# Kernel optimization log

Hardware: AMD Instinct MI355X
Metric: run time of the kernel (lower is better)

## Reference

```python
import jax, jax.numpy as jnp
import numpy as np

N = 100000
E = 1600000
IN_C = 128
HID = 32
H1 = 4
OUT_C = 32
H2 = 1
NEG_SLOPE = 0.2


def setup_inputs() -> dict:
    key = jax.random.key(0)
    ks = jax.random.split(key, 12)
    g = 0.1  # glorot-ish scale
    return {
        "x": jax.random.normal(ks[0], (N, IN_C), jnp.float32),
        "edge_index": jax.random.randint(ks[1], (2, E), 0, N, jnp.int64),
        "W1": jax.random.normal(ks[2], (IN_C, H1 * HID), jnp.float32) * g,
        "att_src1": jax.random.normal(ks[3], (H1, HID), jnp.float32) * g,
        "att_dst1": jax.random.normal(ks[4], (H1, HID), jnp.float32) * g,
        "b1": jnp.zeros((H1 * HID,), jnp.float32),
        "W2": jax.random.normal(ks[5], (H1 * HID, H2 * OUT_C), jnp.float32) * g,
        "att_src2": jax.random.normal(ks[6], (H2, OUT_C), jnp.float32) * g,
        "att_dst2": jax.random.normal(ks[7], (H2, OUT_C), jnp.float32) * g,
        "b2": jnp.zeros((H2 * OUT_C,), jnp.float32),
    }


def gat_conv(x, src, dst, W, att_src, att_dst, bias, heads, ch):
    n = x.shape[0]
    h = (x @ W).reshape(n, heads, ch)                      # [N,H,C]
    a_src = jnp.sum(h * att_src, axis=-1)                  # [N,H]
    a_dst = jnp.sum(h * att_dst, axis=-1)                  # [N,H]
    e = jax.nn.leaky_relu(a_src[src] + a_dst[dst], NEG_SLOPE)  # [E,H]
    # segment softmax over destination neighborhoods
    m = jax.ops.segment_max(e, dst, num_segments=n)        # [N,H]
    ex = jnp.exp(e - m[dst])
    denom = jax.ops.segment_sum(ex, dst, num_segments=n)   # [N,H]
    alpha = ex / (denom[dst] + 1e-16)                      # [E,H]
    msg = h[src] * alpha[:, :, None]                       # [E,H,C]
    out = jax.ops.segment_sum(msg, dst, num_segments=n)    # [N,H,C]
    return out.reshape(n, heads * ch) + bias


def reference(x, edge_index, W1, att_src1, att_dst1, b1, W2, att_src2, att_dst2, b2):
    # PyG GATConv add_self_loops=True
    loops = jnp.arange(N, dtype=edge_index.dtype)
    src = jnp.concatenate([edge_index[0], loops])
    dst = jnp.concatenate([edge_index[1], loops])
    # dropout is a no-op at inference
    h = gat_conv(x, src, dst, W1, att_src1, att_dst1, b1, H1, HID)
    h = jax.nn.relu(h)
    out = gat_conv(h, src, dst, W2, att_src2, att_dst2, b2, H2, OUT_C)
    return out
```

## Files before the change

### kernel.cpp

```cpp
#include <hip/hip_runtime.h>
#include <hip/hip_bf16.h>


#define NSLOPE 0.2f
#define GSTRIDE 136
#define NB_MAX 400
#define CHUNK 4096
#define CAP 5632

typedef __attribute__((ext_vector_type(8))) short short8;
typedef __attribute__((ext_vector_type(4))) float floatx4;

__device__ __forceinline__ float leaky(float v) { return v > 0.f ? v : NSLOPE * v; }

__device__ __forceinline__ unsigned short f2bf(float f) {
  __hip_bfloat16 b = __float2bfloat16(f);
  return *reinterpret_cast<unsigned short*>(&b);
}
__device__ __forceinline__ float bf2f(unsigned int u) {
  return __uint_as_float(u << 16);
}
__device__ __forceinline__ unsigned int pack2(float a, float b) {
  return (unsigned int)f2bf(a) | ((unsigned int)f2bf(b) << 16);
}

__global__ __launch_bounds__(256, 2) void fused1_kernel(
    const float* __restrict__ x, const float* __restrict__ W,
    const float* __restrict__ atts, const float* __restrict__ attd,
    unsigned short* __restrict__ h, float* __restrict__ asrc, float* __restrict__ adst,
    int n, int g1blocks,
    const int* __restrict__ ei, int* __restrict__ bincur,
    unsigned int* __restrict__ staging, int E, int ET, int nb) {
  __shared__ __align__(16) unsigned char smem[70656];
  const int tid = threadIdx.x;

  if (blockIdx.x < g1blocks) {
    unsigned short* xs = (unsigned short*)smem;
    unsigned short* wt = (unsigned short*)(smem + 34816);
    float* att_s = (float*)(smem + 69632);
    float* att_d = (float*)(smem + 70144);
    const int row0 = blockIdx.x * 128;

    if (tid < 128) { att_s[tid] = atts[tid]; att_d[tid] = attd[tid]; }

    const float4* w4 = (const float4*)W;
#pragma unroll
    for (int i = 0; i < 16; i++) {
      int idx = tid + i * 256;
      int k = idx >> 5, n0 = (idx & 31) * 4;
      float4 v = w4[idx];
      float vv[4] = {v.x, v.y, v.z, v.w};
#pragma unroll
      for (int jj = 0; jj < 4; jj++) {
        int j = (jj + tid) & 3;
        wt[(n0 + j) * GSTRIDE + k] = f2bf(vv[j]);
      }
    }

    const float4* x4 = (const float4*)x;
#pragma unroll
    for (int i = 0; i < 16; i++) {
      int idx = tid + i * 256;
      int r = idx >> 5, c4 = idx & 31;
      float4 v = make_float4(0.f, 0.f, 0.f, 0.f);
      if (row0 + r < n) v = x4[(size_t)(row0 + r) * 32 + c4];
      unsigned int* p = (unsigned int*)&xs[r * GSTRIDE + c4 * 4];
      p[0] = pack2(v.x, v.y);
      p[1] = pack2(v.z, v.w);
    }
    __syncthreads();

    const int l = tid & 63;
    const int w = tid >> 6;
    const int mrow = l & 15;
    const int q = l >> 4;
    floatx4 acc[2][8];
#pragma unroll
    for (int mt = 0; mt < 2; mt++)
#pragma unroll
      for (int nt = 0; nt < 8; nt++) acc[mt][nt] = (floatx4){0.f, 0.f, 0.f, 0.f};

#pragma unroll
    for (int ks = 0; ks < 4; ks++) {
      const int k0 = ks * 32 + q * 8;
      short8 a0 = *(const short8*)&xs[(w * 32 + mrow) * GSTRIDE + k0];
      short8 a1 = *(const short8*)&xs[(w * 32 + 16 + mrow) * GSTRIDE + k0];
#pragma unroll
      for (int nt = 0; nt < 8; nt++) {
        short8 b = *(const short8*)&wt[(nt * 16 + mrow) * GSTRIDE + k0];
        acc[0][nt] = __builtin_amdgcn_mfma_f32_16x16x32_bf16(a0, b, acc[0][nt], 0, 0, 0);
        acc[1][nt] = __builtin_amdgcn_mfma_f32_16x16x32_bf16(a1, b, acc[1][nt], 0, 0, 0);
      }
    }
    __syncthreads();

#pragma unroll
    for (int mt = 0; mt < 2; mt++)
#pragma unroll
      for (int nt = 0; nt < 8; nt++)
#pragma unroll
        for (int i = 0; i < 4; i++) {
          int r = w * 32 + mt * 16 + q * 4 + i;
          xs[r * GSTRIDE + nt * 16 + mrow] = f2bf(acc[mt][nt][i]);
        }
    __syncthreads();

#pragma unroll
    for (int i = 0; i < 8; i++) {
      int idx = tid + i * 256;
      int r = idx >> 4, c8 = (idx & 15) * 8;
      if (row0 + r < n) {
        unsigned int* p = (unsigned int*)&xs[r * GSTRIDE + c8];
        uint4 v = make_uint4(p[0], p[1], p[2], p[3]);
        *(uint4*)(h + (size_t)(row0 + r) * 128 + c8) = v;
      }
    }

#pragma unroll
    for (int rr = 0; rr < 2; rr++) {
      int row = (tid >> 2) + rr * 64;
      int head = tid & 3;
      float ss = 0.f, sd = 0.f;
#pragma unroll
      for (int c = 0; c < 32; c++) {
        int cr = (c + tid) & 31;
        float hv = bf2f(xs[row * GSTRIDE + head * 32 + cr]);
        ss += hv * att_s[head * 32 + cr];
        sd += hv * att_d[head * 32 + cr];
      }
      if (row0 + row < n) {
        asrc[(size_t)(row0 + row) * 4 + head] = ss;
        adst[(size_t)(row0 + row) * 4 + head] = sd;
      }
    }
  } else {
    int* hist  = (int*)smem;
    int* run   = (int*)(smem + 1600);
    int* rbase = (int*)(smem + 3200);
    const int base = (blockIdx.x - g1blocks) * CHUNK;
    for (int i = tid; i < nb; i += 256) { hist[i] = 0; run[i] = 0; }
    __syncthreads();
    int se[16], de[16];
#pragma unroll
    for (int j = 0; j < 16; j++) {
      int idx = base + j * 256 + tid;
      if (idx < ET) {
        if (idx < E) { se[j] = ei[idx]; de[j] = ei[E + idx]; }
        else         { se[j] = de[j] = idx - E; }
        atomicAdd(&hist[de[j] >> 8], 1);
      } else de[j] = -1;
    }
    __syncthreads();
    for (int i = tid; i < nb; i += 256)
      rbase[i] = hist[i] ? (i * CAP + atomicAdd(&bincur[i], hist[i])) : 0;
    __syncthreads();
#pragma unroll
    for (int j = 0; j < 16; j++) {
      if (de[j] >= 0) {
        int b = de[j] >> 8;
        int ofs = atomicAdd(&run[b], 1);
        staging[(size_t)rbase[b] + ofs] =
            (unsigned)se[j] | ((unsigned)(de[j] & 255) << 17);
      }
    }
  }
}

__global__ __launch_bounds__(256) void binB_kernel(const unsigned int* __restrict__ staging,
                                                   const int* __restrict__ bincur,
                                                   int* __restrict__ rowbeg,
                                                   int* __restrict__ rowend,
                                                   int* __restrict__ bucket, int n) {
  __shared__ int cnt[256];
  __shared__ int cur[256];
  const int b = blockIdx.x;
  const int t = threadIdx.x;
  const int d0 = b << 8;
  const int nd = min(256, n - d0);
  const int base = b * CAP;
  const int rcnt = bincur[b];
  cnt[t] = 0;
  __syncthreads();
  for (int j = t; j < rcnt; j += 256) {
    unsigned int r = staging[(size_t)base + j];
    atomicAdd(&cnt[r >> 17], 1);
  }
  __syncthreads();
  int v = cnt[t];
  cur[t] = v;
  __syncthreads();
  for (int off = 1; off < 256; off <<= 1) {
    int add = (t >= off) ? cur[t - off] : 0;
    __syncthreads();
    cur[t] += add;
    __syncthreads();
  }
  int start = base + cur[t] - v;
  if (t < nd) { rowbeg[d0 + t] = start; rowend[d0 + t] = start + v; }
  __syncthreads();
  cur[t] = start;
  __syncthreads();
  for (int j = t; j < rcnt; j += 256) {
    unsigned int r = staging[(size_t)base + j];
    int pos = atomicAdd(&cur[r >> 17], 1);
    bucket[pos] = (int)(r & 0x1FFFFu);
  }
}

__global__ __launch_bounds__(256) void g1_kernel(const int* __restrict__ rowbeg,
                                                 const int* __restrict__ rowend,
                                                 const int* __restrict__ bucket,
                                                 const float* __restrict__ asrc,
                                                 const float* __restrict__ adst,
                                                 const unsigned int* __restrict__ h,
                                                 unsigned short* __restrict__ agg,
                                                 int n) {
  const int lane = threadIdx.x & 63;
  const int g = lane >> 3;
  const int l8 = lane & 7;
  const int head = l8 >> 1;
  const int d = blockIdx.x * 4 + (threadIdx.x >> 6);
  if (d >= n) return;
  const float ad = adst[(size_t)d * 4 + head];
  const int beg = rowbeg[d], end = rowend[d];
  float num[16];
#pragma unroll
  for (int j = 0; j < 16; j++) num[j] = 0.f;
  float den = 0.f;

  int i = beg + g;
  if (i < end) {
    int s = bucket[i];
    for (;;) {
      float a = asrc[(size_t)s * 4 + head];
      const uint4* hp = (const uint4*)(h + (size_t)s * 64 + l8 * 8);
      uint4 h0 = hp[0];
      uint4 h1v = hp[1];
      int i2 = i + 8;
      int s2 = (i2 < end) ? bucket[i2] : 0;
      float w = __expf(leaky(a + ad));
      den += w;
      num[0]  += w * bf2f(h0.x & 0xffffu);  num[1]  += w * bf2f(h0.x >> 16);
      num[2]  += w * bf2f(h0.y & 0xffffu);  num[3]  += w * bf2f(h0.y >> 16);
      num[4]  += w * bf2f(h0.z & 0xffffu);  num[5]  += w * bf2f(h0.z >> 16);
      num[6]  += w * bf2f(h0.w & 0xffffu);  num[7]  += w * bf2f(h0.w >> 16);
      num[8]  += w * bf2f(h1v.x & 0xffffu); num[9]  += w * bf2f(h1v.x >> 16);
      num[10] += w * bf2f(h1v.y & 0xffffu); num[11] += w * bf2f(h1v.y >> 16);
      num[12] += w * bf2f(h1v.z & 0xffffu); num[13] += w * bf2f(h1v.z >> 16);
      num[14] += w * bf2f(h1v.w & 0xffffu); num[15] += w * bf2f(h1v.w >> 16);
      if (i2 >= end) break;
      i = i2; s = s2;
    }
  }
#pragma unroll
  for (int j = 0; j < 16; j++) {
    num[j] += __shfl_xor(num[j], 8, 64);
    num[j] += __shfl_xor(num[j], 16, 64);
    num[j] += __shfl_xor(num[j], 32, 64);
  }
  den += __shfl_xor(den, 8, 64);
  den += __shfl_xor(den, 16, 64);
  den += __shfl_xor(den, 32, 64);
  if (g == 0) {
    float inv = 1.f / (den + 1e-16f);
    unsigned short* p = agg + (size_t)d * 128 + l8 * 16;
    uint4 o0, o1;
    o0.x = pack2(num[0] * inv, num[1] * inv);
    o0.y = pack2(num[2] * inv, num[3] * inv);
    o0.z = pack2(num[4] * inv, num[5] * inv);
    o0.w = pack2(num[6] * inv, num[7] * inv);
    o1.x = pack2(num[8] * inv, num[9] * inv);
    o1.y = pack2(num[10] * inv, num[11] * inv);
    o1.z = pack2(num[12] * inv, num[13] * inv);
    o1.w = pack2(num[14] * inv, num[15] * inv);
    *(uint4*)p = o0;
    *(uint4*)(p + 8) = o1;
  }
}

__global__ __launch_bounds__(256, 2) void gemm2_kernel(const unsigned short* __restrict__ agg1,
                                                       const float* __restrict__ b1,
                                                       const float* __restrict__ W,
                                                       const float* __restrict__ atts,
                                                       const float* __restrict__ attd,
                                                       unsigned short* __restrict__ h2,
                                                       float* __restrict__ asrc,
                                                       float* __restrict__ adst, int n) {
  __shared__ __align__(16) unsigned short xs[128 * GSTRIDE];
  __shared__ __align__(16) unsigned short wt[32 * GSTRIDE];
  __shared__ __align__(16) unsigned short hs[128 * 36];
  __shared__ float att_s[32], att_d[32];
  const int tid = threadIdx.x;
  const int row0 = blockIdx.x * 128;

  if (tid < 32) { att_s[tid] = atts[tid]; att_d[tid] = attd[tid]; }

  const float4* w4 = (const float4*)W;
#pragma unroll
  for (int i = 0; i < 4; i++) {
    int idx = tid + i * 256;
    int k = idx >> 3, n0 = (idx & 7) * 4;
    float4 v = w4[idx];
    float vv[4] = {v.x, v.y, v.z, v.w};
#pragma unroll
    for (int jj = 0; jj < 4; jj++) {
      int j = (jj + tid) & 3;
      wt[(n0 + j) * GSTRIDE + k] = f2bf(vv[j]);
    }
  }

  const uint4* a4 = (const uint4*)agg1;
#pragma unroll
  for (int i = 0; i < 8; i++) {
    int idx = tid + i * 256;
    int r = idx >> 4, c8 = (idx & 15) * 8;
    uint4 v = make_uint4(0, 0, 0, 0);
    if (row0 + r < n) v = a4[(size_t)(row0 + r) * 16 + (idx & 15)];
    unsigned int* p = (unsigned int*)&xs[r * GSTRIDE + c8];
    unsigned int vw[4] = {v.x, v.y, v.z, v.w};
#pragma unroll
    for (int j = 0; j < 4; j++) {
      float lo = fmaxf(bf2f(vw[j] & 0xffffu) + b1[c8 + j * 2], 0.f);
      float hi = fmaxf(bf2f(vw[j] >> 16) + b1[c8 + j * 2 + 1], 0.f);
      p[j] = pack2(lo, hi);
    }
  }
  __syncthreads();

  const int l = tid & 63;
  const int w = tid >> 6;
  const int mrow = l & 15;
  const int q = l >> 4;
  floatx4 acc[2][2];
#pragma unroll
  for (int mt = 0; mt < 2; mt++)
#pragma unroll
    for (int nt = 0; nt < 2; nt++) acc[mt][nt] = (floatx4){0.f, 0.f, 0.f, 0.f};

#pragma unroll
  for (int ks = 0; ks < 4; ks++) {
    const int k0 = ks * 32 + q * 8;
    short8 a0 = *(const short8*)&xs[(w * 32 + mrow) * GSTRIDE + k0];
    short8 a1 = *(const short8*)&xs[(w * 32 + 16 + mrow) * GSTRIDE + k0];
#pragma unroll
    for (int nt = 0; nt < 2; nt++) {
      short8 b = *(const short8*)&wt[(nt * 16 + mrow) * GSTRIDE + k0];
      acc[0][nt] = __builtin_amdgcn_mfma_f32_16x16x32_bf16(a0, b, acc[0][nt], 0, 0, 0);
      acc[1][nt] = __builtin_amdgcn_mfma_f32_16x16x32_bf16(a1, b, acc[1][nt], 0, 0, 0);
    }
  }

#pragma unroll
  for (int mt = 0; mt < 2; mt++)
#pragma unroll
    for (int nt = 0; nt < 2; nt++)
#pragma unroll
      for (int i = 0; i < 4; i++) {
        int r = w * 32 + mt * 16 + q * 4 + i;
        hs[r * 36 + nt * 16 + mrow] = f2bf(acc[mt][nt][i]);
      }
  __syncthreads();

#pragma unroll
  for (int i = 0; i < 4; i++) {
    int idx = tid + i * 256;
    int r = idx >> 3, c4 = (idx & 7) * 4;
    if (row0 + r < n) {
      unsigned int* p = (unsigned int*)&hs[r * 36 + c4];
      *(uint2*)(h2 + (size_t)(row0 + r) * 32 + c4) = make_uint2(p[0], p[1]);
    }
  }

  if (tid < 128) {
    int row = tid;
    float ss = 0.f, sd = 0.f;
#pragma unroll
    for (int c = 0; c < 32; c++) {
      int cr = (c + tid) & 31;
      float hv = bf2f(hs[row * 36 + cr]);
      ss += hv * att_s[cr];
      sd += hv * att_d[cr];
    }
    if (row0 + row < n) { asrc[row0 + row] = ss; adst[row0 + row] = sd; }
  }
}

__global__ __launch_bounds__(256) void g2_kernel(const int* __restrict__ rowbeg,
                                                 const int* __restrict__ rowend,
                                                 const int* __restrict__ bucket,
                                                 const float* __restrict__ asrc,
                                                 const float* __restrict__ adst,
                                                 const unsigned int* __restrict__ h2,
                                                 const float* __restrict__ b2,
                                                 float* __restrict__ out, int n) {
  const int lane = threadIdx.x & 63;
  const int g = lane >> 3;
  const int l8 = lane & 7;
  const int d = blockIdx.x * 4 + (threadIdx.x >> 6);
  if (d >= n) return;
  const float ad = adst[d];
  const int beg = rowbeg[d], end = rowend[d];
  float num[4];
#pragma unroll
  for (int j = 0; j < 4; j++) num[j] = 0.f;
  float den = 0.f;

  int i = beg + g;
  if (i < end) {
    int s = bucket[i];
    for (;;) {
      float a = asrc[s];
      uint2 hv = *(const uint2*)(h2 + (size_t)s * 16 + l8 * 2);
      int i2 = i + 8;
      int s2 = (i2 < end) ? bucket[i2] : 0;
      float w = __expf(leaky(a + ad));
      den += w;
      num[0] += w * bf2f(hv.x & 0xffffu); num[1] += w * bf2f(hv.x >> 16);
      num[2] += w * bf2f(hv.y & 0xffffu); num[3] += w * bf2f(hv.y >> 16);
      if (i2 >= end) break;
      i = i2; s = s2;
    }
  }
#pragma unroll
  for (int j = 0; j < 4; j++) {
    num[j] += __shfl_xor(num[j], 8, 64);
    num[j] += __shfl_xor(num[j], 16, 64);
    num[j] += __shfl_xor(num[j], 32, 64);
  }
  den += __shfl_xor(den, 8, 64);
  den += __shfl_xor(den, 16, 64);
  den += __shfl_xor(den, 32, 64);
  if (g == 0) {
    float inv = 1.f / (den + 1e-16f);
    float4 bb = ((const float4*)b2)[l8];
    *(float4*)(out + (size_t)d * 32 + l8 * 4) =
        make_float4(num[0] * inv + bb.x, num[1] * inv + bb.y,
                    num[2] * inv + bb.z, num[3] * inv + bb.w);
  }
}

extern "C" void kernel_launch(void* const* d_in, const int* in_sizes, int n_in,
                              void* d_out, int out_size, void* d_ws, size_t ws_size,
                              hipStream_t stream) {
  const float* x = (const float*)d_in[0];
  const int* ei = (const int*)d_in[1];
  const float* W1 = (const float*)d_in[2];
  const float* atts1 = (const float*)d_in[3];
  const float* attd1 = (const float*)d_in[4];
  const float* b1 = (const float*)d_in[5];
  const float* W2 = (const float*)d_in[6];
  const float* atts2 = (const float*)d_in[7];
  const float* attd2 = (const float*)d_in[8];
  const float* b2 = (const float*)d_in[9];
  float* out = (float*)d_out;

  const int N = in_sizes[0] / 128;
  const int E = in_sizes[1] / 2;
  const int ET = E + N;
  const int NB = (N + 255) >> 8;
  const int NCH = (ET + CHUNK - 1) / CHUNK;
  const int G1B = (N + 127) / 128;

  float* wsf = (float*)d_ws;
  float* asrc1 = wsf;
  float* adst1 = asrc1 + (size_t)N * 4;
  float* asrc2 = adst1 + (size_t)N * 4;
  float* adst2 = asrc2 + (size_t)N;
  unsigned short* agg1 = (unsigned short*)(adst2 + (size_t)N);
  unsigned short* h1 = agg1 + (size_t)N * 128;
  unsigned short* h2 = h1;
  int* rowbeg = (int*)(h1 + (size_t)N * 128);
  int* rowend = rowbeg + N;
  int* bucket = rowend + N;
  unsigned int* staging = (unsigned int*)(bucket + (size_t)NB * CAP);
  int* bincur = (int*)(staging + (size_t)NB * CAP);

  hipMemsetAsync(bincur, 0, NB * sizeof(int), stream);
  fused1_kernel<<<G1B + NCH, 256, 0, stream>>>(x, W1, atts1, attd1, h1, asrc1, adst1,
                                               N, G1B, ei, bincur, staging, E, ET, NB);
  binB_kernel<<<NB, 256, 0, stream>>>(staging, bincur, rowbeg, rowend, bucket, N);
  g1_kernel<<<(N + 3) / 4, 256, 0, stream>>>(rowbeg, rowend, bucket, asrc1, adst1,
                                             (const unsigned int*)h1, agg1, N);
  gemm2_kernel<<<(N + 127) / 128, 256, 0, stream>>>(agg1, b1, W2, atts2, attd2,
                                                    h2, asrc2, adst2, N);
  g2_kernel<<<(N + 3) / 4, 256, 0, stream>>>(rowbeg, rowend, bucket, asrc2, adst2,
                                             (const unsigned int*)h2, b2, out, N);
}
```

Baseline: 290.0 us.

## Fuse layer-1 aggregation with layer-2 GEMM in one 1024-thread kernel

Merges the layer-1 neighbor aggregation kernel and the layer-2 projection GEMM into one kernel. Each 1024-thread block aggregates 128 destination rows straight into shared memory, applying bias and ReLU there, then runs the MFMA GEMM and attention dot products. This removes the agg1 round trip through global memory and one launch. It costs a block-wide barrier that waits on the slowest (highest-degree) row. Large shared memory per block may also limit occupancy and latency hiding for the gather-heavy aggregation.

```diff
diff --git a/kernel.cpp b/kernel.cpp
--- a/kernel.cpp
+++ b/kernel.cpp
@@ -207,181 +207,138 @@
   }
 }
 
-__global__ __launch_bounds__(256) void g1_kernel(const int* __restrict__ rowbeg,
-                                                 const int* __restrict__ rowend,
-                                                 const int* __restrict__ bucket,
-                                                 const float* __restrict__ asrc,
-                                                 const float* __restrict__ adst,
-                                                 const unsigned int* __restrict__ h,
-                                                 unsigned short* __restrict__ agg,
-                                                 int n) {
-  const int lane = threadIdx.x & 63;
+__global__ __launch_bounds__(1024, 8) void g1f_kernel(
+    const int* __restrict__ rowbeg, const int* __restrict__ rowend,
+    const int* __restrict__ bucket,
+    const float* __restrict__ asrc, const float* __restrict__ adst,
+    const unsigned int* __restrict__ h,
+    const float* __restrict__ b1,
+    const float* __restrict__ W2,
+    const float* __restrict__ atts2, const float* __restrict__ attd2,
+    unsigned short* __restrict__ h2,
+    float* __restrict__ asrc2, float* __restrict__ adst2, int n) {
+  __shared__ __align__(16) unsigned short xs[128 * GSTRIDE];
+  __shared__ __align__(16) unsigned short wt[32 * GSTRIDE];
+  __shared__ __align__(16) unsigned short hs[128 * 36];
+  __shared__ float b1s[128];
+  __shared__ float att_s[32], att_d[32];
+  const int tid = threadIdx.x;
+  const int row0 = blockIdx.x * 128;
+
+  {
+    int k = tid >> 3, n0 = (tid & 7) * 4;
+    float4 v = ((const float4*)W2)[tid];
+    float vv[4] = {v.x, v.y, v.z, v.w};
+#pragma unroll
+    for (int jj = 0; jj < 4; jj++) {
+      int j = (jj + tid) & 3;
+      wt[(n0 + j) * GSTRIDE + k] = f2bf(vv[j]);
+    }
+  }
+  if (tid < 128) b1s[tid] = b1[tid];
+  else if (tid < 160) att_s[tid - 128] = atts2[tid - 128];
+  else if (tid < 192) att_d[tid - 160] = attd2[tid - 160];
+  __syncthreads();
+
+  const int wv = tid >> 6;
+  const int lane = tid & 63;
   const int g = lane >> 3;
   const int l8 = lane & 7;
   const int head = l8 >> 1;
-  const int d = blockIdx.x * 4 + (threadIdx.x >> 6);
-  if (d >= n) return;
-  const float ad = adst[(size_t)d * 4 + head];
-  const int beg = rowbeg[d], end = rowend[d];
-  float num[16];
-#pragma unroll
-  for (int j = 0; j < 16; j++) num[j] = 0.f;
-  float den = 0.f;
-
-  int i = beg + g;
-  if (i < end) {
-    int s = bucket[i];
-    for (;;) {
-      float a = asrc[(size_t)s * 4 + head];
-      const uint4* hp = (const uint4*)(h + (size_t)s * 64 + l8 * 8);
-      uint4 h0 = hp[0];
-      uint4 h1v = hp[1];
-      int i2 = i + 8;
-      int s2 = (i2 < end) ? bucket[i2] : 0;
-      float w = __expf(leaky(a + ad));
-      den += w;
-      num[0]  += w * bf2f(h0.x & 0xffffu);  num[1]  += w * bf2f(h0.x >> 16);
-      num[2]  += w * bf2f(h0.y & 0xffffu);  num[3]  += w * bf2f(h0.y >> 16);
-      num[4]  += w * bf2f(h0.z & 0xffffu);  num[5]  += w * bf2f(h0.z >> 16);
-      num[6]  += w * bf2f(h0.w & 0xffffu);  num[7]  += w * bf2f(h0.w >> 16);
-      num[8]  += w * bf2f(h1v.x & 0xffffu); num[9]  += w * bf2f(h1v.x >> 16);
-      num[10] += w * bf2f(h1v.y & 0xffffu); num[11] += w * bf2f(h1v.y >> 16);
-      num[12] += w * bf2f(h1v.z & 0xffffu); num[13] += w * bf2f(h1v.z >> 16);
-      num[14] += w * bf2f(h1v.w & 0xffffu); num[15] += w * bf2f(h1v.w >> 16);
-      if (i2 >= end) break;
-      i = i2; s = s2;
-    }
-  }
-#pragma unroll
-  for (int j = 0; j < 16; j++) {
-    num[j] += __shfl_xor(num[j], 8, 64);
-    num[j] += __shfl_xor(num[j], 16, 64);
-    num[j] += __shfl_xor(num[j], 32, 64);
-  }
-  den += __shfl_xor(den, 8, 64);
-  den += __shfl_xor(den, 16, 64);
-  den += __shfl_xor(den, 32, 64);
-  if (g == 0) {
-    float inv = 1.f / (den + 1e-16f);
-    unsigned short* p = agg + (size_t)d * 128 + l8 * 16;
-    uint4 o0, o1;
-    o0.x = pack2(num[0] * inv, num[1] * inv);
-    o0.y = pack2(num[2] * inv, num[3] * inv);
-    o0.z = pack2(num[4] * inv, num[5] * inv);
-    o0.w = pack2(num[6] * inv, num[7] * inv);
-    o1.x = pack2(num[8] * inv, num[9] * inv);
-    o1.y = pack2(num[10] * inv, num[11] * inv);
-    o1.z = pack2(num[12] * inv, num[13] * inv);
-    o1.w = pack2(num[14] * inv, num[15] * inv);
-    *(uint4*)p = o0;
-    *(uint4*)(p + 8) = o1;
-  }
-}
-
-__global__ __launch_bounds__(256, 2) void gemm2_kernel(const unsigned short* __restrict__ agg1,
-                                                       const float* __restrict__ b1,
-                                                       const float* __restrict__ W,
-                                                       const float* __restrict__ atts,
-                                                       const float* __restrict__ attd,
-                                                       unsigned short* __restrict__ h2,
-                                                       float* __restrict__ asrc,
-                                                       float* __restrict__ adst, int n) {
-  __shared__ __align__(16) unsigned short xs[128 * GSTRIDE];
-  __shared__ __align__(16) unsigned short wt[32 * GSTRIDE];
-  __shared__ __align__(16) unsigned short hs[128 * 36];
-  __shared__ float att_s[32], att_d[32];
-  const int tid = threadIdx.x;
-  const int row0 = blockIdx.x * 128;
-
-  if (tid < 32) { att_s[tid] = atts[tid]; att_d[tid] = attd[tid]; }
-
-  const float4* w4 = (const float4*)W;
-#pragma unroll
-  for (int i = 0; i < 4; i++) {
-    int idx = tid + i * 256;
-    int k = idx >> 3, n0 = (idx & 7) * 4;
-    float4 v = w4[idx];
-    float vv[4] = {v.x, v.y, v.z, v.w};
-#pragma unroll
-    for (int jj = 0; jj < 4; jj++) {
-      int j = (jj + tid) & 3;
-      wt[(n0 + j) * GSTRIDE + k] = f2bf(vv[j]);
-    }
-  }
-
-  const uint4* a4 = (const uint4*)agg1;
-#pragma unroll
-  for (int i = 0; i < 8; i++) {
-    int idx = tid + i * 256;
-    int r = idx >> 4, c8 = (idx & 15) * 8;
-    uint4 v = make_uint4(0, 0, 0, 0);
-    if (row0 + r < n) v = a4[(size_t)(row0 + r) * 16 + (idx & 15)];
-    unsigned int* p = (unsigned int*)&xs[r * GSTRIDE + c8];
-    unsigned int vw[4] = {v.x, v.y, v.z, v.w};
-#pragma unroll
-    for (int j = 0; j < 4; j++) {
-      float lo = fmaxf(bf2f(vw[j] & 0xffffu) + b1[c8 + j * 2], 0.f);
-      float hi = fmaxf(bf2f(vw[j] >> 16) + b1[c8 + j * 2 + 1], 0.f);
-      p[j] = pack2(lo, hi);
-    }
-  }
-  __syncthreads();
-
-  const int l = tid & 63;
-  const int w = tid >> 6;
-  const int mrow = l & 15;
-  const int q = l >> 4;
-  floatx4 acc[2][2];
-#pragma unroll
-  for (int mt = 0; mt < 2; mt++)
-#pragma unroll
-    for (int nt = 0; nt < 2; nt++) acc[mt][nt] = (floatx4){0.f, 0.f, 0.f, 0.f};
-
-#pragma unroll
-  for (int ks = 0; ks < 4; ks++) {
-    const int k0 = ks * 32 + q * 8;
-    short8 a0 = *(const short8*)&xs[(w * 32 + mrow) * GSTRIDE + k0];
-    short8 a1 = *(const short8*)&xs[(w * 32 + 16 + mrow) * GSTRIDE + k0];
-#pragma unroll
-    for (int nt = 0; nt < 2; nt++) {
+  for (int dd = wv; dd < 128; dd += 16) {
+    const int d = row0 + dd;
+    if (d < n) {
+      const float ad = adst[(size_t)d * 4 + head];
+      const int beg = rowbeg[d], end = rowend[d];
+      float num[16];
+#pragma unroll
+      for (int j = 0; j < 16; j++) num[j] = 0.f;
+      float den = 0.f;
+
+      int i = beg + g;
+      if (i < end) {
+        int s = bucket[i];
+        for (;;) {
+          float a = asrc[(size_t)s * 4 + head];
+          const uint4* hp = (const uint4*)(h + (size_t)s * 64 + l8 * 8);
+          uint4 h0 = hp[0];
+          uint4 h1v = hp[1];
+          int i2 = i + 8;
+          int s2 = (i2 < end) ? bucket[i2] : 0;
+          float w = __expf(leaky(a + ad));
+          den += w;
+          num[0]  += w * bf2f(h0.x & 0xffffu);  num[1]  += w * bf2f(h0.x >> 16);
+          num[2]  += w * bf2f(h0.y & 0xffffu);  num[3]  += w * bf2f(h0.y >> 16);
+          num[4]  += w * bf2f(h0.z & 0xffffu);  num[5]  += w * bf2f(h0.z >> 16);
+          num[6]  += w * bf2f(h0.w & 0xffffu);  num[7]  += w * bf2f(h0.w >> 16);
+          num[8]  += w * bf2f(h1v.x & 0xffffu); num[9]  += w * bf2f(h1v.x >> 16);
+          num[10] += w * bf2f(h1v.y & 0xffffu); num[11] += w * bf2f(h1v.y >> 16);
+          num[12] += w * bf2f(h1v.z & 0xffffu); num[13] += w * bf2f(h1v.z >> 16);
+          num[14] += w * bf2f(h1v.w & 0xffffu); num[15] += w * bf2f(h1v.w >> 16);
+          if (i2 >= end) break;
+          i = i2; s = s2;
+        }
+      }
+#pragma unroll
+      for (int j = 0; j < 16; j++) {
+        num[j] += __shfl_xor(num[j], 8, 64);
+        num[j] += __shfl_xor(num[j], 16, 64);
+        num[j] += __shfl_xor(num[j], 32, 64);
+      }
+      den += __shfl_xor(den, 8, 64);
+      den += __shfl_xor(den, 16, 64);
+      den += __shfl_xor(den, 32, 64);
+      if (g == 0) {
+        float inv = 1.f / (den + 1e-16f);
+        unsigned int* p = (unsigned int*)&xs[dd * GSTRIDE + l8 * 16];
+#pragma unroll
+        for (int j = 0; j < 8; j++) {
+          float lo = fmaxf(num[j * 2] * inv + b1s[l8 * 16 + j * 2], 0.f);
+          float hi = fmaxf(num[j * 2 + 1] * inv + b1s[l8 * 16 + j * 2 + 1], 0.f);
+          p[j] = pack2(lo, hi);
+        }
+      }
+    }
+  }
+  __syncthreads();
+
+  {
+    const int mrow = lane & 15;
+    const int q = lane >> 4;
+    const int mt = wv >> 1;
+    const int nt = wv & 1;
+    floatx4 acc = (floatx4){0.f, 0.f, 0.f, 0.f};
+#pragma unroll
+    for (int ks = 0; ks < 4; ks++) {
+      const int k0 = ks * 32 + q * 8;
+      short8 a = *(const short8*)&xs[(mt * 16 + mrow) * GSTRIDE + k0];
       short8 b = *(const short8*)&wt[(nt * 16 + mrow) * GSTRIDE + k0];
-      acc[0][nt] = __builtin_amdgcn_mfma_f32_16x16x32_bf16(a0, b, acc[0][nt], 0, 0, 0);
-      acc[1][nt] = __builtin_amdgcn_mfma_f32_16x16x32_bf16(a1, b, acc[1][nt], 0, 0, 0);
-    }
-  }
-
-#pragma unroll
-  for (int mt = 0; mt < 2; mt++)
-#pragma unroll
-    for (int nt = 0; nt < 2; nt++)
-#pragma unroll
-      for (int i = 0; i < 4; i++) {
-        int r = w * 32 + mt * 16 + q * 4 + i;
-        hs[r * 36 + nt * 16 + mrow] = f2bf(acc[mt][nt][i]);
-      }
-  __syncthreads();
-
-#pragma unroll
-  for (int i = 0; i < 4; i++) {
-    int idx = tid + i * 256;
-    int r = idx >> 3, c4 = (idx & 7) * 4;
+      acc = __builtin_amdgcn_mfma_f32_16x16x32_bf16(a, b, acc, 0, 0, 0);
+    }
+#pragma unroll
+    for (int i = 0; i < 4; i++)
+      hs[(mt * 16 + q * 4 + i) * 36 + nt * 16 + mrow] = f2bf(acc[i]);
+  }
+  __syncthreads();
+
+  {
+    int r = tid >> 3, c4 = (tid & 7) * 4;
     if (row0 + r < n) {
       unsigned int* p = (unsigned int*)&hs[r * 36 + c4];
       *(uint2*)(h2 + (size_t)(row0 + r) * 32 + c4) = make_uint2(p[0], p[1]);
     }
   }
-
-  if (tid < 128) {
-    int row = tid;
+  if (tid < 128 && row0 + tid < n) {
     float ss = 0.f, sd = 0.f;
 #pragma unroll
     for (int c = 0; c < 32; c++) {
       int cr = (c + tid) & 31;
-      float hv = bf2f(hs[row * 36 + cr]);
+      float hv = bf2f(hs[tid * 36 + cr]);
       ss += hv * att_s[cr];
       sd += hv * att_d[cr];
     }
-    if (row0 + row < n) { asrc[row0 + row] = ss; adst[row0 + row] = sd; }
+    asrc2[row0 + tid] = ss;
+    adst2[row0 + tid] = sd;
   }
 }
 
@@ -466,10 +423,9 @@
   float* adst1 = asrc1 + (size_t)N * 4;
   float* asrc2 = adst1 + (size_t)N * 4;
   float* adst2 = asrc2 + (size_t)N;
-  unsigned short* agg1 = (unsigned short*)(adst2 + (size_t)N);
-  unsigned short* h1 = agg1 + (size_t)N * 128;
-  unsigned short* h2 = h1;
-  int* rowbeg = (int*)(h1 + (size_t)N * 128);
+  unsigned short* h1 = (unsigned short*)(adst2 + (size_t)N);
+  unsigned short* h2 = h1 + (size_t)N * 128;
+  int* rowbeg = (int*)(h2 + (size_t)N * 32);
   int* rowend = rowbeg + N;
   int* bucket = rowend + N;
   unsigned int* staging = (unsigned int*)(bucket + (size_t)NB * CAP);
@@ -479,10 +435,9 @@
   fused1_kernel<<<G1B + NCH, 256, 0, stream>>>(x, W1, atts1, attd1, h1, asrc1, adst1,
                                                N, G1B, ei, bincur, staging, E, ET, NB);
   binB_kernel<<<NB, 256, 0, stream>>>(staging, bincur, rowbeg, rowend, bucket, N);
-  g1_kernel<<<(N + 3) / 4, 256, 0, stream>>>(rowbeg, rowend, bucket, asrc1, adst1,
-                                             (const unsigned int*)h1, agg1, N);
-  gemm2_kernel<<<(N + 127) / 128, 256, 0, stream>>>(agg1, b1, W2, atts2, attd2,
-                                                    h2, asrc2, adst2, N);
+  g1f_kernel<<<G1B, 1024, 0, stream>>>(rowbeg, rowend, bucket, asrc1, adst1,
+                                       (const unsigned int*)h1, b1, W2, atts2, attd2,
+                                       h2, asrc2, adst2, N);
   g2_kernel<<<(N + 3) / 4, 256, 0, stream>>>(rowbeg, rowend, bucket, asrc2, adst2,
                                              (const unsigned int*)h2, b2, out, N);
 }
```

New measurement: 299.5 us. 3.3% more time.
